# Optimization experiments

Hardware: AMD Instinct MI355X
Metric: run time of the kernel (lower is better)

## Reference

```python
import jax, jax.numpy as jnp
import numpy as np
from jax.ops import segment_sum

N = 20000; IN = 256; HID = 256; Z = 64; DEC_H = 64; E = 120000; NEG = 5
BETA = 1.0; LN_EPS = 1e-5; TAU_MIN = 1e-4


def setup_inputs() -> dict:
    rng = np.random.default_rng(0)
    a = rng.integers(0, N, E)
    b = (a + 1 + rng.integers(0, N - 1, E)) % N  # guarantees a != b
    lo, hi = np.minimum(a, b), np.maximum(a, b)
    pos_edge = jnp.asarray(np.stack([lo, hi]), dtype=jnp.int32)          # [2,E], i<j single copy
    edge_index = jnp.asarray(np.stack([np.concatenate([lo, hi]),
                                       np.concatenate([hi, lo])]), dtype=jnp.int32)  # [2,2E] undirected
    neg_edge = jnp.asarray(rng.integers(0, N, (2, NEG * E)), dtype=jnp.int32)
    ks = jax.random.split(jax.random.key(0), 12)
    p = lambda i, shape, s=0.02: (jax.random.normal(ks[i], shape, jnp.float32) * s)
    return dict(
        x=p(0, (N, IN), 1.0), eps=p(1, (N, Z), 1.0),
        edge_index=edge_index, pos_edge=pos_edge, neg_edge=neg_edge,
        W1=p(2, (IN, HID)), b1=jnp.zeros((HID,), jnp.float32),
        g1=jnp.ones((HID,), jnp.float32), bt1=jnp.zeros((HID,), jnp.float32),
        Wmu=p(3, (HID, Z)), bmu=jnp.zeros((Z,), jnp.float32),
        Wlv=p(4, (HID, Z)), blv=jnp.zeros((Z,), jnp.float32),
        Wd1=p(5, (Z, Z)), bd1=jnp.zeros((Z,), jnp.float32),
        Wd2=p(6, (Z, Z)), bd2=jnp.zeros((Z,), jnp.float32),
        Wa=p(7, (4 * Z, DEC_H)), ba=jnp.zeros((DEC_H,), jnp.float32),
        Wb=p(8, (DEC_H, 1)), bb=jnp.zeros((1,), jnp.float32),
        tau=jnp.array(1.0, jnp.float32))


def _gcn_plain(h, src, dst, W, b):
    # GCNConv(add_self_loops=False, normalize=False): unnormalized scatter-add
    m = h @ W                                   # [N,F]
    return segment_sum(m[src], dst, num_segments=N) + b


def _gcn_norm(h, src, dst, W, b):
    # GCNConv defaults: self loops + symmetric normalization
    loops = jnp.arange(N, dtype=src.dtype)
    s = jnp.concatenate([src, loops]); d = jnp.concatenate([dst, loops])
    deg = segment_sum(jnp.ones_like(d, jnp.float32), d, num_segments=N)  # in-degree incl self
    dis = jax.lax.rsqrt(jnp.maximum(deg, 1.0))
    norm = dis[s] * dis[d]                      # [Emsg+N]
    m = h @ W
    return segment_sum(m[s] * norm[:, None], d, num_segments=N) + b


def _layernorm(h, g, bt):
    mu = jnp.mean(h, axis=-1, keepdims=True)
    var = jnp.mean((h - mu) ** 2, axis=-1, keepdims=True)
    return (h - mu) * jax.lax.rsqrt(var + LN_EPS) * g + bt


def _forward(x, eps, edge_index, pos_edge, neg_edge, W1, b1, g1, bt1, Wmu, bmu,
             Wlv, blv, Wd1, bd1, Wd2, bd2, Wa, ba, Wb, bb, tau):
    src, dst = edge_index[0], edge_index[1]
    # Encoder (dropout inactive: eval-mode reference)
    h1 = jax.nn.relu(_layernorm(_gcn_plain(x, src, dst, W1, b1), g1, bt1))
    mu = _gcn_plain(h1, src, dst, Wmu, bmu)
    logvar = _gcn_plain(h1, src, dst, Wlv, blv)
    z = mu + eps * jnp.exp(0.5 * logvar)
    # EdgeDecoder: 2 normalized GCN passes over positive (i<j) edges only
    ps, pd = pos_edge[0], pos_edge[1]
    h = jax.nn.relu(_gcn_norm(z, ps, pd, Wd1, bd1))
    h = jax.nn.relu(_gcn_norm(h, ps, pd, Wd2, bd2))
    # edge gather -> concat features -> MLP
    eu = jnp.concatenate([pos_edge[0], neg_edge[0]])
    ev = jnp.concatenate([pos_edge[1], neg_edge[1]])
    hu, hv = h[eu], h[ev]                        # [Ep+En, Z]
    phi = jnp.concatenate([hu, hv, jnp.abs(hu - hv), hu * hv], axis=-1)  # [Ep+En, 4Z]
    logits = (jax.nn.relu(phi @ Wa + ba) @ Wb + bb)[:, 0]
    logits = logits / jnp.clip(tau, TAU_MIN)
    # weighted BCE-with-logits; pos_weight = #neg/#pos = NEG
    n_pos = pos_edge.shape[1]; n_neg = neg_edge.shape[1]
    labels = jnp.concatenate([jnp.ones((n_pos,), jnp.float32), jnp.zeros((n_neg,), jnp.float32)])
    pw = jnp.float32(n_neg) / jnp.float32(n_pos)
    recon = -jnp.mean(pw * labels * jax.nn.log_sigmoid(logits)
                      + (1.0 - labels) * jax.nn.log_sigmoid(-logits))
    kl = -0.5 * jnp.mean(1.0 + logvar - mu ** 2 - jnp.exp(logvar))
    loss = recon + BETA * kl
    return loss, recon, kl


def reference(x, eps, edge_index, pos_edge, neg_edge, W1, b1, g1, bt1, Wmu, bmu,
              Wlv, blv, Wd1, bd1, Wd2, bd2, Wa, ba, Wb, bb, tau):
    return _forward(x, eps, edge_index, pos_edge, neg_edge, W1, b1, g1, bt1, Wmu,
                    bmu, Wlv, blv, Wd1, bd1, Wd2, bd2, Wa, ba, Wb, bb, tau)
```

## Files before the change

### kernel.cpp

```cpp
#include <hip/hip_runtime.h>
#include <hip/hip_bf16.h>
#include <math.h>

#define N_NODES 20000
#define E2      240000
#define EP      120000
#define ENEG    600000
#define ETOT    720000
#define NTILE   11250
#define EMLP_BLOCKS 1024

#define WA_B  64
#define W1T_B 256
#define WML_B 128
#define UV_B  2813
#define HA_B  938
#define HP_B  469
#define FA_B  938
#define FP_B  469
#define DIS_B 79

typedef __attribute__((ext_vector_type(8))) short bf16x8;
typedef __attribute__((ext_vector_type(4))) float f32x4;

__device__ __forceinline__ float logsigf(float x) {
    return fminf(x, 0.0f) - log1pf(expf(-fabsf(x)));
}

__device__ __forceinline__ unsigned short f2bf(float f) {
    unsigned u = __float_as_uint(f);
    u += 0x7FFF + ((u >> 16) & 1);
    return (unsigned short)(u >> 16);
}

__device__ __forceinline__ float bflo(unsigned u) { return __uint_as_float(u << 16); }
__device__ __forceinline__ float bfhi(unsigned u) { return __uint_as_float(u & 0xFFFF0000u); }

__device__ __forceinline__ void store_out(float v, float* p) { *p = v; }
__device__ __forceinline__ void store_out(float v, unsigned short* p) { *p = f2bf(v); }
__device__ __forceinline__ float load_in(const float* p) { return *p; }
__device__ __forceinline__ float load_in(const unsigned short* p) {
    return __uint_as_float(((unsigned)*p) << 16);
}

__device__ __forceinline__ bf16x8 make_ad(int4 a, int4 b) {
    const unsigned* pa = (const unsigned*)&a;
    const unsigned* pb = (const unsigned*)&b;
    union { unsigned u[4]; bf16x8 v; } out;
#pragma unroll
    for (int i = 0; i < 4; ++i) {
        const float lo = fabsf(bflo(pa[i]) - bflo(pb[i]));
        const float hi = fabsf(bfhi(pa[i]) - bfhi(pb[i]));
        union { __hip_bfloat162 h; unsigned u; } c;
        c.h = __float22bfloat162_rn(float2{lo, hi});
        out.u[i] = c.u;
    }
    return out.v;
}

__device__ __forceinline__ bf16x8 make_pr(int4 a, int4 b) {
    const unsigned* pa = (const unsigned*)&a;
    const unsigned* pb = (const unsigned*)&b;
    union { unsigned u[4]; bf16x8 v; } out;
#pragma unroll
    for (int i = 0; i < 4; ++i) {
        const float lo = bflo(pa[i]) * bflo(pb[i]);
        const float hi = bfhi(pa[i]) * bfhi(pb[i]);
        union { __hip_bfloat162 h; unsigned u; } c;
        c.h = __float22bfloat162_rn(float2{lo, hi});
        out.u[i] = c.u;
    }
    return out.v;
}

__global__ void k_prep_csr(const float* __restrict__ Wa, unsigned short* __restrict__ WaT,
                           const float* __restrict__ W1, unsigned short* __restrict__ W1T,
                           const float* __restrict__ Wmu, const float* __restrict__ Wlv,
                           unsigned short* __restrict__ WmlT,
                           const int* __restrict__ pos, const int* __restrict__ neg,
                           int2* __restrict__ uv,
                           const int* __restrict__ e_dst, int* __restrict__ cntA,
                           const int* __restrict__ pd, int* __restrict__ cntP) {
    const int b = blockIdx.x, tid = threadIdx.x;
    if (b < WA_B) {
        const int idx = b * 256 + tid;
        const int n = idx >> 8, kp = idx & 255;
        const int part = kp >> 6;
        const int d = ((kp >> 3) & 3) * 16 + ((kp >> 5) & 1) * 8 + (kp & 7);
        WaT[idx] = f2bf(Wa[(part * 64 + d) * 64 + n]);
    } else if (b < WA_B + W1T_B) {
        const int idx = (b - WA_B) * 256 + tid;
        const int n = idx >> 8, k = idx & 255;
        W1T[idx] = f2bf(W1[k * 256 + n]);
    } else if (b < WA_B + W1T_B + WML_B) {
        const int idx = (b - WA_B - W1T_B) * 256 + tid;
        const int n = idx >> 8, k = idx & 255;
        const float* W = (n & 1) ? Wlv : Wmu;
        WmlT[idx] = f2bf(W[k * 64 + (n >> 1)]);
    } else if (b < WA_B + W1T_B + WML_B + UV_B) {
        const int j = (b - WA_B - W1T_B - WML_B) * 256 + tid;
        if (j < ETOT) {
            int u, v;
            if (j < EP) { u = pos[j]; v = pos[EP + j]; }
            else        { u = neg[j - EP]; v = neg[ENEG + (j - EP)]; }
            uv[j] = make_int2(u, v);
        }
    } else if (b < WA_B + W1T_B + WML_B + UV_B + HA_B) {
        const int e = (b - WA_B - W1T_B - WML_B - UV_B) * 256 + tid;
        if (e < E2) atomicAdd(&cntA[e_dst[e]], 1);
    } else {
        const int e = (b - WA_B - W1T_B - WML_B - UV_B - HA_B) * 256 + tid;
        if (e < EP) atomicAdd(&cntP[pd[e]], 1);
    }
}

__global__ __launch_bounds__(1024) void k_scan2(int* __restrict__ cntA, int* __restrict__ rsA,
                                                int* __restrict__ cntP, int* __restrict__ rsP) {
    int* cnt = blockIdx.x ? cntP : cntA;
    int* rs  = blockIdx.x ? rsP  : rsA;
    int* cur = cnt;
    const int n = N_NODES;
    __shared__ int wexc[16];
    __shared__ int s_carry, s_tot;
    const int tid = threadIdx.x, lane = tid & 63, wid = tid >> 6;
    if (tid == 0) s_carry = 0;
    __syncthreads();
    for (int base = 0; base < n; base += 1024) {
        const int i = base + tid;
        const int v = (i < n) ? cnt[i] : 0;
        int x = v;
#pragma unroll
        for (int d = 1; d < 64; d <<= 1) {
            const int t = __shfl_up(x, d, 64);
            if (lane >= d) x += t;
        }
        if (lane == 63) wexc[wid] = x;
        __syncthreads();
        if (tid == 0) {
            int a = 0;
#pragma unroll
            for (int k = 0; k < 16; ++k) { const int t = wexc[k]; wexc[k] = a; a += t; }
            s_tot = a;
        }
        __syncthreads();
        const int excl = s_carry + wexc[wid] + x - v;
        if (i < n) { rs[i] = excl; cur[i] = excl; }
        __syncthreads();
        if (tid == 0) s_carry += s_tot;
        __syncthreads();
    }
    if (tid == 0) rs[n] = s_carry;
}

__global__ void k_finish_csr(const int* __restrict__ e_src, const int* __restrict__ e_dst,
                             int* __restrict__ curA, int* __restrict__ adjA,
                             const int* __restrict__ ps, const int* __restrict__ pd,
                             int* __restrict__ curP, int* __restrict__ adjP,
                             const int* __restrict__ rsP, float* __restrict__ dis) {
    const int b = blockIdx.x, tid = threadIdx.x;
    if (b < FA_B) {
        const int e = b * 256 + tid;
        if (e < E2) {
            const int p = atomicAdd(&curA[e_dst[e]], 1);
            adjA[p] = e_src[e];
        }
    } else if (b < FA_B + FP_B) {
        const int e = (b - FA_B) * 256 + tid;
        if (e < EP) {
            const int p = atomicAdd(&curP[pd[e]], 1);
            adjP[p] = ps[e];
        }
    } else {
        const int i = (b - FA_B - FP_B) * 256 + tid;
        if (i < N_NODES) dis[i] = rsqrtf((float)(rsP[i + 1] - rsP[i] + 1));
    }
}

__global__ __launch_bounds__(256) void k_mm_xW1_mfma(const float* __restrict__ x,
                                                     const unsigned short* __restrict__ W1T,
                                                     unsigned short* __restrict__ m1) {
    __shared__ unsigned short sA[32 * 264];
    const int tid = threadIdx.x;
    const int w = tid >> 6, lane = tid & 63;
    const int l15 = lane & 15, quad = lane >> 4;
    const int mb = blockIdx.x >> 2, nb = blockIdx.x & 3;

    for (int i = tid; i < 2048; i += 256) {
        const int row = i >> 6, kc = (i & 63) << 2;
        const float4 xv = *(const float4*)&x[((long)mb * 32 + row) * 256 + kc];
        union { unsigned short s[4]; unsigned long long ll; } pk;
        pk.s[0] = f2bf(xv.x); pk.s[1] = f2bf(xv.y);
        pk.s[2] = f2bf(xv.z); pk.s[3] = f2bf(xv.w);
        *(unsigned long long*)&sA[row * 264 + kc] = pk.ll;
    }

    bf16x8 breg[8];
#pragma unroll
    for (int ks = 0; ks < 8; ++ks)
        breg[ks] = *(const bf16x8*)&W1T[((nb * 64 + w * 16 + l15) << 8) + ks * 32 + quad * 8];
    __syncthreads();

    f32x4 acc[2];
    acc[0] = (f32x4){0.f,0.f,0.f,0.f};
    acc[1] = (f32x4){0.f,0.f,0.f,0.f};
#pragma unroll
    for (int ks = 0; ks < 8; ++ks) {
#pragma unroll
        for (int st = 0; st < 2; ++st) {
            const bf16x8 af = *(const bf16x8*)&sA[(st * 16 + l15) * 264 + ks * 32 + quad * 8];
            acc[st] = __builtin_amdgcn_mfma_f32_16x16x32_bf16(af, breg[ks], acc[st], 0, 0, 0);
        }
    }
#pragma unroll
    for (int st = 0; st < 2; ++st)
#pragma unroll
        for (int r = 0; r < 4; ++r)
            m1[((long)mb * 32 + st * 16 + quad * 4 + r) * 256 + nb * 64 + w * 16 + l15] =
                f2bf(acc[st][r]);
}

__global__ __launch_bounds__(256) void k_gather_ln(const unsigned short* __restrict__ m1,
                                                   const int* __restrict__ rs,
                                                   const int* __restrict__ adj,
                                                   const float* __restrict__ b1,
                                                   const float* __restrict__ g1,
                                                   const float* __restrict__ bt1,
                                                   unsigned short* __restrict__ h1) {
    const int wid = threadIdx.x >> 6, lane = threadIdx.x & 63;
    const int n = blockIdx.x * 4 + wid;
    const int beg = rs[n], end = rs[n + 1];
    float4 a0 = {0.f,0.f,0.f,0.f}, a1 = {0.f,0.f,0.f,0.f};
    float4 a2 = {0.f,0.f,0.f,0.f}, a3 = {0.f,0.f,0.f,0.f};
    int j = beg;
    for (; j + 3 < end; j += 4) {
        const int s0 = adj[j], s1 = adj[j + 1], s2 = adj[j + 2], s3 = adj[j + 3];
        const uint2 u0 = *(const uint2*)(m1 + (long)s0 * 256 + lane * 4);
        const uint2 u1 = *(const uint2*)(m1 + (long)s1 * 256 + lane * 4);
        const uint2 u2 = *(const uint2*)(m1 + (long)s2 * 256 + lane * 4);
        const uint2 u3 = *(const uint2*)(m1 + (long)s3 * 256 + lane * 4);
        a0.x += bflo(u0.x); a0.y += bfhi(u0.x); a0.z += bflo(u0.y); a0.w += bfhi(u0.y);
        a1.x += bflo(u1.x); a1.y += bfhi(u1.x); a1.z += bflo(u1.y); a1.w += bfhi(u1.y);
        a2.x += bflo(u2.x); a2.y += bfhi(u2.x); a2.z += bflo(u2.y); a2.w += bfhi(u2.y);
        a3.x += bflo(u3.x); a3.y += bfhi(u3.x); a3.z += bflo(u3.y); a3.w += bfhi(u3.y);
    }
    for (; j < end; ++j) {
        const int s0 = adj[j];
        const uint2 u = *(const uint2*)(m1 + (long)s0 * 256 + lane * 4);
        a0.x += bflo(u.x); a0.y += bfhi(u.x); a0.z += bflo(u.y); a0.w += bfhi(u.y);
    }
    float4 v;
    const float4 b = *(const float4*)(b1 + lane * 4);
    v.x = (a0.x + a1.x) + (a2.x + a3.x) + b.x;
    v.y = (a0.y + a1.y) + (a2.y + a3.y) + b.y;
    v.z = (a0.z + a1.z) + (a2.z + a3.z) + b.z;
    v.w = (a0.w + a1.w) + (a2.w + a3.w) + b.w;
    float s  = v.x + v.y + v.z + v.w;
    float sq = v.x * v.x + v.y * v.y + v.z * v.z + v.w * v.w;
    for (int o = 32; o > 0; o >>= 1) {
        s  += __shfl_xor(s, o, 64);
        sq += __shfl_xor(sq, o, 64);
    }
    const float mean = s * (1.0f / 256.0f);
    const float var  = sq * (1.0f / 256.0f) - mean * mean;
    const float rsv = rsqrtf(var + 1e-5f);
    const float4 g  = *(const float4*)(g1 + lane * 4);
    const float4 bt = *(const float4*)(bt1 + lane * 4);
    union { unsigned short sh[4]; unsigned long long ll; } pk;
    pk.sh[0] = f2bf(fmaxf((v.x - mean) * rsv * g.x + bt.x, 0.f));
    pk.sh[1] = f2bf(fmaxf((v.y - mean) * rsv * g.y + bt.y, 0.f));
    pk.sh[2] = f2bf(fmaxf((v.z - mean) * rsv * g.z + bt.z, 0.f));
    pk.sh[3] = f2bf(fmaxf((v.w - mean) * rsv * g.w + bt.w, 0.f));
    *(unsigned long long*)&h1[(long)n * 256 + lane * 4] = pk.ll;
}

__global__ __launch_bounds__(256) void k_mm_hml_mfma(const unsigned short* __restrict__ h1,
                                                     const unsigned short* __restrict__ WmlT,
                                                     unsigned short* __restrict__ hml) {
    __shared__ unsigned short sA[32 * 264];
    const int tid = threadIdx.x;
    const int w = tid >> 6, lane = tid & 63;
    const int l15 = lane & 15, quad = lane >> 4;
    const int mb = blockIdx.x >> 1, nb = blockIdx.x & 1;

    for (int i = tid; i < 1024; i += 256) {
        const int row = i >> 5, kc = (i & 31) << 3;
        *(int4*)&sA[row * 264 + kc] = *(const int4*)&h1[((long)mb * 32 + row) * 256 + kc];
    }

    bf16x8 breg[8];
#pragma unroll
    for (int ks = 0; ks < 8; ++ks)
        breg[ks] = *(const bf16x8*)&WmlT[((nb * 64 + w * 16 + l15) << 8) + ks * 32 + quad * 8];
    __syncthreads();

    f32x4 acc[2];
    acc[0] = (f32x4){0.f,0.f,0.f,0.f};
    acc[1] = (f32x4){0.f,0.f,0.f,0.f};
#pragma unroll
    for (int ks = 0; ks < 8; ++ks) {
#pragma unroll
        for (int st = 0; st < 2; ++st) {
            const bf16x8 af = *(const bf16x8*)&sA[(st * 16 + l15) * 264 + ks * 32 + quad * 8];
            acc[st] = __builtin_amdgcn_mfma_f32_16x16x32_bf16(af, breg[ks], acc[st], 0, 0, 0);
        }
    }
#pragma unroll
    for (int st = 0; st < 2; ++st)
#pragma unroll
        for (int r = 0; r < 4; ++r)
            hml[((long)mb * 32 + st * 16 + quad * 4 + r) * 128 + nb * 64 + w * 16 + l15] =
                f2bf(acc[st][r]);
}

__global__ __launch_bounds__(256) void k_gather_mulv(const unsigned short* __restrict__ hml,
                                                     const int* __restrict__ rs,
                                                     const int* __restrict__ adj,
                                                     const float* __restrict__ bmu,
                                                     const float* __restrict__ blv,
                                                     const float* __restrict__ eps,
                                                     unsigned short* __restrict__ z,
                                                     double* __restrict__ kl_part) {
    __shared__ double sKL[4];
    const int wid = threadIdx.x >> 6, lane = threadIdx.x & 63;
    const int n = blockIdx.x * 4 + wid;
    const int beg = rs[n], end = rs[n + 1];
    float m0 = 0.f, m1_ = 0.f, m2 = 0.f, m3 = 0.f;
    float l0 = 0.f, l1 = 0.f, l2 = 0.f, l3 = 0.f;
    int j = beg;
    for (; j + 3 < end; j += 4) {
        const int s0 = adj[j], s1 = adj[j + 1], s2 = adj[j + 2], s3 = adj[j + 3];
        const unsigned u0 = *(const unsigned*)(hml + (long)s0 * 128 + lane * 2);
        const unsigned u1 = *(const unsigned*)(hml + (long)s1 * 128 + lane * 2);
        const unsigned u2 = *(const unsigned*)(hml + (long)s2 * 128 + lane * 2);
        const unsigned u3 = *(const unsigned*)(hml + (long)s3 * 128 + lane * 2);
        m0 += bflo(u0); l0 += bfhi(u0);
        m1_ += bflo(u1); l1 += bfhi(u1);
        m2 += bflo(u2); l2 += bfhi(u2);
        m3 += bflo(u3); l3 += bfhi(u3);
    }
    for (; j < end; ++j) {
        const int s0 = adj[j];
        const unsigned u0 = *(const unsigned*)(hml + (long)s0 * 128 + lane * 2);
        m0 += bflo(u0); l0 += bfhi(u0);
    }
    const float mu = (m0 + m1_) + (m2 + m3) + bmu[lane];
    const float lv = (l0 + l1) + (l2 + l3) + blv[lane];
    z[(long)n * 64 + lane] = f2bf(mu + eps[(long)n * 64 + lane] * expf(0.5f * lv));
    float term = 1.0f + lv - mu * mu - expf(lv);
    for (int o = 32; o > 0; o >>= 1) term += __shfl_xor(term, o, 64);
    if (lane == 0) sKL[wid] = (double)term;
    __syncthreads();
    if (threadIdx.x == 0)
        kl_part[blockIdx.x] = sKL[0] + sKL[1] + sKL[2] + sKL[3];
}

template <typename IN, typename OUT>
__global__ __launch_bounds__(256) void k_dec_fused(const IN* __restrict__ feat,
                                                   const int* __restrict__ rs,
                                                   const int* __restrict__ adj,
                                                   const float* __restrict__ dis,
                                                   const float* __restrict__ Wd,
                                                   const float* __restrict__ bd,
                                                   OUT* __restrict__ out) {
    __shared__ float sW[64 * 64];
    __shared__ float rows[4][64];
    const int tid = threadIdx.x;
    {
        const float4* w4 = (const float4*)Wd;
        float4* sw4 = (float4*)sW;
        for (int i = tid; i < 1024; i += 256) sw4[i] = w4[i];
    }
    const int wid = tid >> 6, lane = tid & 63;
    const int n = blockIdx.x * 4 + wid;
    const int beg = rs[n], end = rs[n + 1];
    float a0 = 0.f, a1 = 0.f, a2 = 0.f, a3 = 0.f;
    int j = beg;
    for (; j + 3 < end; j += 4) {
        const int s0 = adj[j], s1 = adj[j + 1], s2 = adj[j + 2], s3 = adj[j + 3];
        a0 += load_in(&feat[(long)s0 * 64 + lane]) * dis[s0];
        a1 += load_in(&feat[(long)s1 * 64 + lane]) * dis[s1];
        a2 += load_in(&feat[(long)s2 * 64 + lane]) * dis[s2];
        a3 += load_in(&feat[(long)s3 * 64 + lane]) * dis[s3];
    }
    for (; j < end; ++j) {
        const int s0 = adj[j];
        a0 += load_in(&feat[(long)s0 * 64 + lane]) * dis[s0];
    }
    const float dn = dis[n];
    rows[wid][lane] = ((a0 + a1) + (a2 + a3)) * dn
                    + load_in(&feat[(long)n * 64 + lane]) * dn * dn;
    __syncthreads();
    float acc = 0.f;
    for (int k = 0; k < 64; k += 4) {
        const float4 a = *(const float4*)&rows[wid][k];
        acc += a.x * sW[(k+0)*64+lane] + a.y * sW[(k+1)*64+lane]
             + a.z * sW[(k+2)*64+lane] + a.w * sW[(k+3)*64+lane];
    }
    store_out(fmaxf(acc + bd[lane], 0.f), &out[(long)n * 64 + lane]);
}

__global__ __launch_bounds__(256, 2) void k_edge_mlp_mfma(
        const unsigned short* __restrict__ h2bf,
        const int2* __restrict__ uv,
        const unsigned short* __restrict__ WaT,
        const float* __restrict__ ba,
        const float* __restrict__ Wb,
        const float* __restrict__ bb,
        const float* __restrict__ tau,
        double* __restrict__ recon_part) {
    __shared__ double sRed[4];
    const int tid = threadIdx.x;
    const int w = tid >> 6, lane = tid & 63;
    const int l15 = lane & 15, quad = lane >> 4;

    bf16x8 areg[4][8];
#pragma unroll
    for (int nt = 0; nt < 4; ++nt)
#pragma unroll
        for (int ks = 0; ks < 8; ++ks)
            areg[nt][ks] = *(const bf16x8*)&WaT[((nt * 16 + l15) << 8) + ks * 32 + quad * 8];

    const float bb0 = bb[0];
    const float itau = 1.0f / fmaxf(tau[0], 1e-4f);

    float lsum = 0.f;

    int t = blockIdx.x;
    int2 uvp = uv[t * 64 + w * 16 + l15];
    int4 hua = *(const int4*)&h2bf[uvp.x * 64 + quad * 16];
    int4 hub = *(const int4*)&h2bf[uvp.x * 64 + quad * 16 + 8];
    int4 hva = *(const int4*)&h2bf[uvp.y * 64 + quad * 16];
    int4 hvb = *(const int4*)&h2bf[uvp.y * 64 + quad * 16 + 8];

    for (; t < NTILE; t += EMLP_BLOCKS) {
        const int tn = t + EMLP_BLOCKS;
        int2 uvn = uvp;
        if (tn < NTILE) uvn = uv[tn * 64 + w * 16 + l15];

        const bf16x8 fad_a = make_ad(hua, hva);
        const bf16x8 fad_b = make_ad(hub, hvb);
        const bf16x8 fpr_a = make_pr(hua, hva);
        const bf16x8 fpr_b = make_pr(hub, hvb);

        f32x4 acc[4];
#pragma unroll
        for (int nt = 0; nt < 4; ++nt) acc[nt] = (f32x4){0.f, 0.f, 0.f, 0.f};

        const bf16x8 bhu_a = *(const bf16x8*)&hua;
        const bf16x8 bhu_b = *(const bf16x8*)&hub;
        const bf16x8 bhv_a = *(const bf16x8*)&hva;
        const bf16x8 bhv_b = *(const bf16x8*)&hvb;

#pragma unroll
        for (int nt = 0; nt < 4; ++nt) {
            acc[nt] = __builtin_amdgcn_mfma_f32_16x16x32_bf16(areg[nt][0], bhu_a, acc[nt], 0, 0, 0);
            acc[nt] = __builtin_amdgcn_mfma_f32_16x16x32_bf16(areg[nt][1], bhu_b, acc[nt], 0, 0, 0);
            acc[nt] = __builtin_amdgcn_mfma_f32_16x16x32_bf16(areg[nt][2], bhv_a, acc[nt], 0, 0, 0);
            acc[nt] = __builtin_amdgcn_mfma_f32_16x16x32_bf16(areg[nt][3], bhv_b, acc[nt], 0, 0, 0);
            acc[nt] = __builtin_amdgcn_mfma_f32_16x16x32_bf16(areg[nt][4], fad_a, acc[nt], 0, 0, 0);
            acc[nt] = __builtin_amdgcn_mfma_f32_16x16x32_bf16(areg[nt][5], fad_b, acc[nt], 0, 0, 0);
            acc[nt] = __builtin_amdgcn_mfma_f32_16x16x32_bf16(areg[nt][6], fpr_a, acc[nt], 0, 0, 0);
            acc[nt] = __builtin_amdgcn_mfma_f32_16x16x32_bf16(areg[nt][7], fpr_b, acc[nt], 0, 0, 0);
        }

        if (tn < NTILE) {
            hua = *(const int4*)&h2bf[uvn.x * 64 + quad * 16];
            hub = *(const int4*)&h2bf[uvn.x * 64 + quad * 16 + 8];
            hva = *(const int4*)&h2bf[uvn.y * 64 + quad * 16];
            hvb = *(const int4*)&h2bf[uvn.y * 64 + quad * 16 + 8];
        }
        uvp = uvn;

        float s = 0.f;
#pragma unroll
        for (int nt = 0; nt < 4; ++nt) {
            const float4 b4 = *(const float4*)&ba[nt * 16 + quad * 4];
            const float4 w4 = *(const float4*)&Wb[nt * 16 + quad * 4];
            s += fmaxf(acc[nt][0] + b4.x, 0.f) * w4.x
               + fmaxf(acc[nt][1] + b4.y, 0.f) * w4.y
               + fmaxf(acc[nt][2] + b4.z, 0.f) * w4.z
               + fmaxf(acc[nt][3] + b4.w, 0.f) * w4.w;
        }
        s += __shfl_xor(s, 16, 64);
        s += __shfl_xor(s, 32, 64);
        if (lane < 16) {
            const long j = (long)t * 64 + w * 16 + lane;
            const float logit = (s + bb0) * itau;
            lsum += (j < EP) ? 5.0f * logsigf(logit) : logsigf(-logit);
        }
    }

    for (int o = 32; o > 0; o >>= 1) lsum += __shfl_xor(lsum, o, 64);
    if (lane == 0) sRed[w] = (double)lsum;
    __syncthreads();
    if (tid == 0)
        recon_part[blockIdx.x] = sRed[0] + sRed[1] + sRed[2] + sRed[3];
}

__global__ __launch_bounds__(1024) void k_final(const double* __restrict__ kl_part,
                                                const double* __restrict__ recon_part,
                                                float* __restrict__ out) {
    __shared__ double sK[16], sR[16];
    const int tid = threadIdx.x, lane = tid & 63, wid = tid >> 6;
    double kl = 0.0, rc = 0.0;
    for (int i = tid; i < 5000; i += 1024) kl += kl_part[i];
    for (int i = tid; i < EMLP_BLOCKS; i += 1024) rc += recon_part[i];
    for (int o = 32; o > 0; o >>= 1) {
        kl += __shfl_xor(kl, o, 64);
        rc += __shfl_xor(rc, o, 64);
    }
    if (lane == 0) { sK[wid] = kl; sR[wid] = rc; }
    __syncthreads();
    if (tid == 0) {
        double K = 0.0, R = 0.0;
        for (int i = 0; i < 16; ++i) { K += sK[i]; R += sR[i]; }
        const double recon = -R / (double)ETOT;
        const double klv = -0.5 * K / ((double)N_NODES * 64.0);
        out[0] = (float)(recon + klv);
        out[1] = (float)recon;
        out[2] = (float)klv;
    }
}

extern "C" void kernel_launch(void* const* d_in, const int* in_sizes, int n_in,
                              void* d_out, int out_size, void* d_ws, size_t ws_size,
                              hipStream_t stream) {
    const float* x   = (const float*)d_in[0];
    const float* eps = (const float*)d_in[1];
    const int* EI    = (const int*)d_in[2];
    const int* pos   = (const int*)d_in[3];
    const int* neg   = (const int*)d_in[4];
    const float* W1  = (const float*)d_in[5];
    const float* b1  = (const float*)d_in[6];
    const float* g1  = (const float*)d_in[7];
    const float* bt1 = (const float*)d_in[8];
    const float* Wmu = (const float*)d_in[9];
    const float* bmu = (const float*)d_in[10];
    const float* Wlv = (const float*)d_in[11];
    const float* blv = (const float*)d_in[12];
    const float* Wd1 = (const float*)d_in[13];
    const float* bd1 = (const float*)d_in[14];
    const float* Wd2 = (const float*)d_in[15];
    const float* bd2 = (const float*)d_in[16];
    const float* Wa  = (const float*)d_in[17];
    const float* ba  = (const float*)d_in[18];
    const float* Wb  = (const float*)d_in[19];
    const float* bb  = (const float*)d_in[20];
    const float* tau = (const float*)d_in[21];

    const int* e_src = EI;
    const int* e_dst = EI + E2;
    const int* ps = pos;
    const int* pd = pos + EP;

    float* ws = (float*)d_ws;
    unsigned short* m1bf  = (unsigned short*)ws;
    unsigned short* hmlbf = (unsigned short*)ws;
    unsigned short* hdec  = (unsigned short*)(ws + 2560000);
    unsigned short* h2bf = (unsigned short*)(ws + 3840000);
    unsigned short* h1bf = (unsigned short*)(ws + 5120000);
    unsigned short* z    = (unsigned short*)(ws + 10240000);
    float* dis   = ws + 11520000;
    unsigned short* WaT = (unsigned short*)(ws + 11540004);
    int* cntA = (int*)(ws + 11548200);
    int* rsA  = (int*)(ws + 11568200);
    int* adjA = (int*)(ws + 11588204);
    int* cntP = (int*)(ws + 11828204);
    int* rsP  = (int*)(ws + 11848204);
    int* adjP = (int*)(ws + 11868208);
    int2* uv  = (int2*)(ws + 11988208);
    double* kl_part    = (double*)(ws + 13428208);
    double* recon_part = (double*)(ws + 13438208);
    unsigned short* W1T  = (unsigned short*)(ws + 13440256);
    unsigned short* WmlT = (unsigned short*)(ws + 13473024);

    hipMemsetAsync(cntA, 0, N_NODES * 4, stream);
    hipMemsetAsync(cntP, 0, N_NODES * 4, stream);

    k_prep_csr<<<WA_B + W1T_B + WML_B + UV_B + HA_B + HP_B, 256, 0, stream>>>(
        Wa, WaT, W1, W1T, Wmu, Wlv, WmlT, pos, neg, uv, e_dst, cntA, pd, cntP);
    k_scan2<<<2, 1024, 0, stream>>>(cntA, rsA, cntP, rsP);
    k_finish_csr<<<FA_B + FP_B + DIS_B, 256, 0, stream>>>(
        e_src, e_dst, cntA, adjA, ps, pd, cntP, adjP, rsP, dis);

    k_mm_xW1_mfma<<<2500, 256, 0, stream>>>(x, W1T, m1bf);
    k_gather_ln<<<5000, 256, 0, stream>>>(m1bf, rsA, adjA, b1, g1, bt1, h1bf);
    k_mm_hml_mfma<<<1250, 256, 0, stream>>>(h1bf, WmlT, hmlbf);
    k_gather_mulv<<<5000, 256, 0, stream>>>(hmlbf, rsA, adjA, bmu, blv, eps, z, kl_part);

    k_dec_fused<unsigned short, unsigned short><<<5000, 256, 0, stream>>>(
        z, rsP, adjP, dis, Wd1, bd1, hdec);
    k_dec_fused<unsigned short, unsigned short><<<5000, 256, 0, stream>>>(
        hdec, rsP, adjP, dis, Wd2, bd2, h2bf);

    k_edge_mlp_mfma<<<EMLP_BLOCKS, 256, 0, stream>>>(h2bf, uv, WaT, ba, Wb, bb, tau, recon_part);
    k_final<<<1, 1024, 0, stream>>>(kl_part, recon_part, (float*)d_out);
}
```

Before: 333.9 us.

## Switch decoder/edge-MLP to fp16 packed math, parallelize CSR scan, raise occupancy

Stores decoder activations and the Wa weights in fp16 so the edge MLP can build |hu-hv| and hu*hv with packed half2 ops instead of unpacking bf16 to float, and uses f16 MFMA. The single-block-per-array serial scan is replaced by 40 blocks, each recomputing its chunk prefix by reduction, and cursors now live in separate arrays. The edge MLP launch bound is raised to 4 waves per SIMD, and the positive-edge test becomes a per-tile comparison. fp16 gives a narrower range than bf16, which risks overflow or precision differences in the activations.

```diff
diff --git a/kernel.cpp b/kernel.cpp
--- a/kernel.cpp
+++ b/kernel.cpp
@@ -1,5 +1,6 @@
 #include <hip/hip_runtime.h>
 #include <hip/hip_bf16.h>
+#include <hip/hip_fp16.h>
 #include <math.h>
 
 #define N_NODES 20000
@@ -8,7 +9,9 @@
 #define ENEG    600000
 #define ETOT    720000
 #define NTILE   11250
+#define POSTILE 1875
 #define EMLP_BLOCKS 1024
+#define NCHUNK  20
 
 #define WA_B  64
 #define W1T_B 256
@@ -21,6 +24,7 @@
 #define DIS_B 79
 
 typedef __attribute__((ext_vector_type(8))) short bf16x8;
+typedef __attribute__((ext_vector_type(8))) _Float16 f16x8;
 typedef __attribute__((ext_vector_type(4))) float f32x4;
 
 __device__ __forceinline__ float logsigf(float x) {
@@ -33,44 +37,38 @@
     return (unsigned short)(u >> 16);
 }
 
+__device__ __forceinline__ unsigned short f2h(float f) {
+    return __half_as_ushort(__float2half(f));
+}
+
 __device__ __forceinline__ float bflo(unsigned u) { return __uint_as_float(u << 16); }
 __device__ __forceinline__ float bfhi(unsigned u) { return __uint_as_float(u & 0xFFFF0000u); }
 
 __device__ __forceinline__ void store_out(float v, float* p) { *p = v; }
 __device__ __forceinline__ void store_out(float v, unsigned short* p) { *p = f2bf(v); }
+__device__ __forceinline__ void store_out(float v, __half* p) { *p = __float2half(v); }
 __device__ __forceinline__ float load_in(const float* p) { return *p; }
 __device__ __forceinline__ float load_in(const unsigned short* p) {
     return __uint_as_float(((unsigned)*p) << 16);
 }
-
-__device__ __forceinline__ bf16x8 make_ad(int4 a, int4 b) {
-    const unsigned* pa = (const unsigned*)&a;
-    const unsigned* pb = (const unsigned*)&b;
-    union { unsigned u[4]; bf16x8 v; } out;
-#pragma unroll
-    for (int i = 0; i < 4; ++i) {
-        const float lo = fabsf(bflo(pa[i]) - bflo(pb[i]));
-        const float hi = fabsf(bfhi(pa[i]) - bfhi(pb[i]));
-        union { __hip_bfloat162 h; unsigned u; } c;
-        c.h = __float22bfloat162_rn(float2{lo, hi});
-        out.u[i] = c.u;
-    }
-    return out.v;
-}
-
-__device__ __forceinline__ bf16x8 make_pr(int4 a, int4 b) {
-    const unsigned* pa = (const unsigned*)&a;
-    const unsigned* pb = (const unsigned*)&b;
-    union { unsigned u[4]; bf16x8 v; } out;
-#pragma unroll
-    for (int i = 0; i < 4; ++i) {
-        const float lo = bflo(pa[i]) * bflo(pb[i]);
-        const float hi = bfhi(pa[i]) * bfhi(pb[i]);
-        union { __hip_bfloat162 h; unsigned u; } c;
-        c.h = __float22bfloat162_rn(float2{lo, hi});
-        out.u[i] = c.u;
-    }
-    return out.v;
+__device__ __forceinline__ float load_in(const __half* p) { return __half2float(*p); }
+
+union I4H { int4 i; __half2 h[4]; f16x8 f; };
+
+__device__ __forceinline__ f16x8 make_ad16(int4 a, int4 b) {
+    I4H ua, ub, r;
+    ua.i = a; ub.i = b;
+#pragma unroll
+    for (int k = 0; k < 4; ++k) r.h[k] = __habs2(__hsub2(ua.h[k], ub.h[k]));
+    return r.f;
+}
+
+__device__ __forceinline__ f16x8 make_pr16(int4 a, int4 b) {
+    I4H ua, ub, r;
+    ua.i = a; ub.i = b;
+#pragma unroll
+    for (int k = 0; k < 4; ++k) r.h[k] = __hmul2(ua.h[k], ub.h[k]);
+    return r.f;
 }
 
 __global__ void k_prep_csr(const float* __restrict__ Wa, unsigned short* __restrict__ WaT,
@@ -87,7 +85,7 @@
         const int n = idx >> 8, kp = idx & 255;
         const int part = kp >> 6;
         const int d = ((kp >> 3) & 3) * 16 + ((kp >> 5) & 1) * 8 + (kp & 7);
-        WaT[idx] = f2bf(Wa[(part * 64 + d) * 64 + n]);
+        WaT[idx] = f2h(Wa[(part * 64 + d) * 64 + n]);
     } else if (b < WA_B + W1T_B) {
         const int idx = (b - WA_B) * 256 + tid;
         const int n = idx >> 8, k = idx & 255;
@@ -114,42 +112,46 @@
     }
 }
 
-__global__ __launch_bounds__(1024) void k_scan2(int* __restrict__ cntA, int* __restrict__ rsA,
-                                                int* __restrict__ cntP, int* __restrict__ rsP) {
-    int* cnt = blockIdx.x ? cntP : cntA;
-    int* rs  = blockIdx.x ? rsP  : rsA;
-    int* cur = cnt;
-    const int n = N_NODES;
-    __shared__ int wexc[16];
-    __shared__ int s_carry, s_tot;
+__global__ __launch_bounds__(1024) void k_scan_par(const int* __restrict__ cntA,
+                                                   int* __restrict__ rsA,
+                                                   int* __restrict__ curA,
+                                                   const int* __restrict__ cntP,
+                                                   int* __restrict__ rsP,
+                                                   int* __restrict__ curP) {
+    const int arr = blockIdx.x / NCHUNK;
+    const int c   = blockIdx.x % NCHUNK;
+    const int* cnt = arr ? cntP : cntA;
+    int* rs  = arr ? rsP  : rsA;
+    int* cur = arr ? curP : curA;
     const int tid = threadIdx.x, lane = tid & 63, wid = tid >> 6;
-    if (tid == 0) s_carry = 0;
-    __syncthreads();
-    for (int base = 0; base < n; base += 1024) {
-        const int i = base + tid;
-        const int v = (i < n) ? cnt[i] : 0;
-        int x = v;
-#pragma unroll
-        for (int d = 1; d < 64; d <<= 1) {
-            const int t = __shfl_up(x, d, 64);
-            if (lane >= d) x += t;
-        }
-        if (lane == 63) wexc[wid] = x;
-        __syncthreads();
-        if (tid == 0) {
-            int a = 0;
-#pragma unroll
-            for (int k = 0; k < 16; ++k) { const int t = wexc[k]; wexc[k] = a; a += t; }
-            s_tot = a;
-        }
-        __syncthreads();
-        const int excl = s_carry + wexc[wid] + x - v;
-        if (i < n) { rs[i] = excl; cur[i] = excl; }
-        __syncthreads();
-        if (tid == 0) s_carry += s_tot;
-        __syncthreads();
-    }
-    if (tid == 0) rs[n] = s_carry;
+    __shared__ int wred[16];
+
+    int p = 0;
+    for (int i = tid; i < c * 1024; i += 1024) p += cnt[i];
+    for (int o = 32; o > 0; o >>= 1) p += __shfl_xor(p, o, 64);
+    if (lane == 0) wred[wid] = p;
+    __syncthreads();
+    int prefix = 0;
+#pragma unroll
+    for (int k = 0; k < 16; ++k) prefix += wred[k];
+    __syncthreads();
+
+    const int i = c * 1024 + tid;
+    const int v = (i < N_NODES) ? cnt[i] : 0;
+    int x = v;
+#pragma unroll
+    for (int d = 1; d < 64; d <<= 1) {
+        const int t = __shfl_up(x, d, 64);
+        if (lane >= d) x += t;
+    }
+    if (lane == 63) wred[wid] = x;
+    __syncthreads();
+    int wexc = 0, tot = 0;
+#pragma unroll
+    for (int k = 0; k < 16; ++k) { if (k < wid) wexc += wred[k]; tot += wred[k]; }
+    const int excl = prefix + wexc + x - v;
+    if (i < N_NODES) { rs[i] = excl; cur[i] = excl; }
+    if (c == NCHUNK - 1 && tid == 0) rs[N_NODES] = prefix + tot;
 }
 
 __global__ void k_finish_csr(const int* __restrict__ e_src, const int* __restrict__ e_dst,
@@ -399,8 +401,8 @@
     store_out(fmaxf(acc + bd[lane], 0.f), &out[(long)n * 64 + lane]);
 }
 
-__global__ __launch_bounds__(256, 2) void k_edge_mlp_mfma(
-        const unsigned short* __restrict__ h2bf,
+__global__ __launch_bounds__(256, 4) void k_edge_mlp_mfma(
+        const __half* __restrict__ h2,
         const int2* __restrict__ uv,
         const unsigned short* __restrict__ WaT,
         const float* __restrict__ ba,
@@ -413,12 +415,12 @@
     const int w = tid >> 6, lane = tid & 63;
     const int l15 = lane & 15, quad = lane >> 4;
 
-    bf16x8 areg[4][8];
+    f16x8 areg[4][8];
 #pragma unroll
     for (int nt = 0; nt < 4; ++nt)
 #pragma unroll
         for (int ks = 0; ks < 8; ++ks)
-            areg[nt][ks] = *(const bf16x8*)&WaT[((nt * 16 + l15) << 8) + ks * 32 + quad * 8];
+            areg[nt][ks] = *(const f16x8*)&WaT[((nt * 16 + l15) << 8) + ks * 32 + quad * 8];
 
     const float bb0 = bb[0];
     const float itau = 1.0f / fmaxf(tau[0], 1e-4f);
@@ -427,47 +429,47 @@
 
     int t = blockIdx.x;
     int2 uvp = uv[t * 64 + w * 16 + l15];
-    int4 hua = *(const int4*)&h2bf[uvp.x * 64 + quad * 16];
-    int4 hub = *(const int4*)&h2bf[uvp.x * 64 + quad * 16 + 8];
-    int4 hva = *(const int4*)&h2bf[uvp.y * 64 + quad * 16];
-    int4 hvb = *(const int4*)&h2bf[uvp.y * 64 + quad * 16 + 8];
+    int4 hua = *(const int4*)(h2 + (long)uvp.x * 64 + quad * 16);
+    int4 hub = *(const int4*)(h2 + (long)uvp.x * 64 + quad * 16 + 8);
+    int4 hva = *(const int4*)(h2 + (long)uvp.y * 64 + quad * 16);
+    int4 hvb = *(const int4*)(h2 + (long)uvp.y * 64 + quad * 16 + 8);
 
     for (; t < NTILE; t += EMLP_BLOCKS) {
         const int tn = t + EMLP_BLOCKS;
         int2 uvn = uvp;
         if (tn < NTILE) uvn = uv[tn * 64 + w * 16 + l15];
 
-        const bf16x8 fad_a = make_ad(hua, hva);
-        const bf16x8 fad_b = make_ad(hub, hvb);
-        const bf16x8 fpr_a = make_pr(hua, hva);
-        const bf16x8 fpr_b = make_pr(hub, hvb);
+        const f16x8 fad_a = make_ad16(hua, hva);
+        const f16x8 fad_b = make_ad16(hub, hvb);
+        const f16x8 fpr_a = make_pr16(hua, hva);
+        const f16x8 fpr_b = make_pr16(hub, hvb);
 
         f32x4 acc[4];
 #pragma unroll
         for (int nt = 0; nt < 4; ++nt) acc[nt] = (f32x4){0.f, 0.f, 0.f, 0.f};
 
-        const bf16x8 bhu_a = *(const bf16x8*)&hua;
-        const bf16x8 bhu_b = *(const bf16x8*)&hub;
-        const bf16x8 bhv_a = *(const bf16x8*)&hva;
-        const bf16x8 bhv_b = *(const bf16x8*)&hvb;
+        const f16x8 bhu_a = *(const f16x8*)&hua;
+        const f16x8 bhu_b = *(const f16x8*)&hub;
+        const f16x8 bhv_a = *(const f16x8*)&hva;
+        const f16x8 bhv_b = *(const f16x8*)&hvb;
 
 #pragma unroll
         for (int nt = 0; nt < 4; ++nt) {
-            acc[nt] = __builtin_amdgcn_mfma_f32_16x16x32_bf16(areg[nt][0], bhu_a, acc[nt], 0, 0, 0);
-            acc[nt] = __builtin_amdgcn_mfma_f32_16x16x32_bf16(areg[nt][1], bhu_b, acc[nt], 0, 0, 0);
-            acc[nt] = __builtin_amdgcn_mfma_f32_16x16x32_bf16(areg[nt][2], bhv_a, acc[nt], 0, 0, 0);
-            acc[nt] = __builtin_amdgcn_mfma_f32_16x16x32_bf16(areg[nt][3], bhv_b, acc[nt], 0, 0, 0);
-            acc[nt] = __builtin_amdgcn_mfma_f32_16x16x32_bf16(areg[nt][4], fad_a, acc[nt], 0, 0, 0);
-            acc[nt] = __builtin_amdgcn_mfma_f32_16x16x32_bf16(areg[nt][5], fad_b, acc[nt], 0, 0, 0);
-            acc[nt] = __builtin_amdgcn_mfma_f32_16x16x32_bf16(areg[nt][6], fpr_a, acc[nt], 0, 0, 0);
-            acc[nt] = __builtin_amdgcn_mfma_f32_16x16x32_bf16(areg[nt][7], fpr_b, acc[nt], 0, 0, 0);
+            acc[nt] = __builtin_amdgcn_mfma_f32_16x16x32_f16(areg[nt][0], bhu_a, acc[nt], 0, 0, 0);
+            acc[nt] = __builtin_amdgcn_mfma_f32_16x16x32_f16(areg[nt][1], bhu_b, acc[nt], 0, 0, 0);
+            acc[nt] = __builtin_amdgcn_mfma_f32_16x16x32_f16(areg[nt][2], bhv_a, acc[nt], 0, 0, 0);
+            acc[nt] = __builtin_amdgcn_mfma_f32_16x16x32_f16(areg[nt][3], bhv_b, acc[nt], 0, 0, 0);
+            acc[nt] = __builtin_amdgcn_mfma_f32_16x16x32_f16(areg[nt][4], fad_a, acc[nt], 0, 0, 0);
+            acc[nt] = __builtin_amdgcn_mfma_f32_16x16x32_f16(areg[nt][5], fad_b, acc[nt], 0, 0, 0);
+            acc[nt] = __builtin_amdgcn_mfma_f32_16x16x32_f16(areg[nt][6], fpr_a, acc[nt], 0, 0, 0);
+            acc[nt] = __builtin_amdgcn_mfma_f32_16x16x32_f16(areg[nt][7], fpr_b, acc[nt], 0, 0, 0);
         }
 
         if (tn < NTILE) {
-            hua = *(const int4*)&h2bf[uvn.x * 64 + quad * 16];
-            hub = *(const int4*)&h2bf[uvn.x * 64 + quad * 16 + 8];
-            hva = *(const int4*)&h2bf[uvn.y * 64 + quad * 16];
-            hvb = *(const int4*)&h2bf[uvn.y * 64 + quad * 16 + 8];
+            hua = *(const int4*)(h2 + (long)uvn.x * 64 + quad * 16);
+            hub = *(const int4*)(h2 + (long)uvn.x * 64 + quad * 16 + 8);
+            hva = *(const int4*)(h2 + (long)uvn.y * 64 + quad * 16);
+            hvb = *(const int4*)(h2 + (long)uvn.y * 64 + quad * 16 + 8);
         }
         uvp = uvn;
 
@@ -484,9 +486,9 @@
         s += __shfl_xor(s, 16, 64);
         s += __shfl_xor(s, 32, 64);
         if (lane < 16) {
-            const long j = (long)t * 64 + w * 16 + lane;
             const float logit = (s + bb0) * itau;
-            lsum += (j < EP) ? 5.0f * logsigf(logit) : logsigf(-logit);
+            const bool isPos = (t < POSTILE);
+            lsum += isPos ? 5.0f * logsigf(logit) : logsigf(-logit);
         }
     }
 
@@ -556,8 +558,8 @@
     float* ws = (float*)d_ws;
     unsigned short* m1bf  = (unsigned short*)ws;
     unsigned short* hmlbf = (unsigned short*)ws;
-    unsigned short* hdec  = (unsigned short*)(ws + 2560000);
-    unsigned short* h2bf = (unsigned short*)(ws + 3840000);
+    __half* hdec = (__half*)(ws + 2560000);
+    __half* h2   = (__half*)(ws + 3840000);
     unsigned short* h1bf = (unsigned short*)(ws + 5120000);
     unsigned short* z    = (unsigned short*)(ws + 10240000);
     float* dis   = ws + 11520000;
@@ -573,26 +575,28 @@
     double* recon_part = (double*)(ws + 13438208);
     unsigned short* W1T  = (unsigned short*)(ws + 13440256);
     unsigned short* WmlT = (unsigned short*)(ws + 13473024);
+    int* curA = (int*)(ws + 13489408);
+    int* curP = (int*)(ws + 13509408);
 
     hipMemsetAsync(cntA, 0, N_NODES * 4, stream);
     hipMemsetAsync(cntP, 0, N_NODES * 4, stream);
 
     k_prep_csr<<<WA_B + W1T_B + WML_B + UV_B + HA_B + HP_B, 256, 0, stream>>>(
         Wa, WaT, W1, W1T, Wmu, Wlv, WmlT, pos, neg, uv, e_dst, cntA, pd, cntP);
-    k_scan2<<<2, 1024, 0, stream>>>(cntA, rsA, cntP, rsP);
+    k_scan_par<<<2 * NCHUNK, 1024, 0, stream>>>(cntA, rsA, curA, cntP, rsP, curP);
     k_finish_csr<<<FA_B + FP_B + DIS_B, 256, 0, stream>>>(
-        e_src, e_dst, cntA, adjA, ps, pd, cntP, adjP, rsP, dis);
+        e_src, e_dst, curA, adjA, ps, pd, curP, adjP, rsP, dis);
 
     k_mm_xW1_mfma<<<2500, 256, 0, stream>>>(x, W1T, m1bf);
     k_gather_ln<<<5000, 256, 0, stream>>>(m1bf, rsA, adjA, b1, g1, bt1, h1bf);
     k_mm_hml_mfma<<<1250, 256, 0, stream>>>(h1bf, WmlT, hmlbf);
     k_gather_mulv<<<5000, 256, 0, stream>>>(hmlbf, rsA, adjA, bmu, blv, eps, z, kl_part);
 
-    k_dec_fused<unsigned short, unsigned short><<<5000, 256, 0, stream>>>(
+    k_dec_fused<unsigned short, __half><<<5000, 256, 0, stream>>>(
         z, rsP, adjP, dis, Wd1, bd1, hdec);
-    k_dec_fused<unsigned short, unsigned short><<<5000, 256, 0, stream>>>(
-        hdec, rsP, adjP, dis, Wd2, bd2, h2bf);
-
-    k_edge_mlp_mfma<<<EMLP_BLOCKS, 256, 0, stream>>>(h2bf, uv, WaT, ba, Wb, bb, tau, recon_part);
+    k_dec_fused<__half, __half><<<5000, 256, 0, stream>>>(
+        hdec, rsP, adjP, dis, Wd2, bd2, h2);
+
+    k_edge_mlp_mfma<<<EMLP_BLOCKS, 256, 0, stream>>>(h2, uv, WaT, ba, Wb, bb, tau, recon_part);
     k_final<<<1, 1024, 0, stream>>>(kl_part, recon_part, (float*)d_out);
 }
```

New measurement: 462.0 us. +38.4%, slower.
